# Optimization experiments

Hardware: AMD Instinct MI355X
Metric: run time of the kernel (lower is better)

The kernel has to match this reference:

```python
import jax, jax.numpy as jnp
import numpy as np

H = 2880      # hidden_size
NH = 64       # num query heads
NKV = 8       # num kv heads
D = 64        # head_dim
G = NH // NKV # GQA group size
W = 128       # sliding window (keys per query, incl. self)
THETA = 150000.0
N = 1024      # tokens


def setup_inputs() -> dict:
    key = jax.random.key(0)
    k0, k1, k2, k3 = jax.random.split(key, 4)
    hidden_states = jax.random.normal(k0, (N, H), jnp.float32)
    Wqkv = jax.random.normal(k1, (H, (NH + 2 * NKV) * D), jnp.float32) * (H ** -0.5)
    Wo = jax.random.normal(k2, (NH * D, H), jnp.float32) * ((NH * D) ** -0.5)
    sinks = jax.random.normal(k3, (NH,), jnp.float32)
    positions = jnp.arange(N, dtype=jnp.int64)
    return {"hidden_states": hidden_states, "Wqkv": Wqkv, "Wo": Wo,
            "sinks": sinks, "positions": positions}


def _rope(x, pos):
    # NeoX-style rotary over full head_dim. x: [n, h, D], pos: [n]
    half = D // 2
    inv_freq = 1.0 / (THETA ** (jnp.arange(half, dtype=jnp.float32) / half))
    ang = pos[:, None].astype(jnp.float32) * inv_freq          # [n, half]
    cos = jnp.cos(ang)[:, None, :]
    sin = jnp.sin(ang)[:, None, :]
    x1, x2 = x[..., :half], x[..., half:]
    return jnp.concatenate([x1 * cos - x2 * sin, x2 * cos + x1 * sin], axis=-1)


def reference(hidden_states, Wqkv, Wo, sinks, positions):
    n = hidden_states.shape[0]
    qkv = hidden_states @ Wqkv
    q, k, v = jnp.split(qkv, [NH * D, NH * D + NKV * D], axis=-1)
    q = _rope(q.reshape(n, NH, D), positions)   # [n, NH, D]
    k = _rope(k.reshape(n, NKV, D), positions)  # [n, NKV, D]
    v = v.reshape(n, NKV, D)

    # Sliding-window key indices: query i attends keys j in [i-W+1, i]
    idx = positions[:, None] - (W - 1) + jnp.arange(W)[None, :]  # [n, W]
    valid = idx >= 0
    idx = jnp.clip(idx, 0, n - 1)
    k_win = k[idx]  # [n, W, NKV, D]
    v_win = v[idx]  # [n, W, NKV, D]

    qg = q.reshape(n, NKV, G, D)
    scores = jnp.einsum('nkgd,nwkd->nkgw', qg, k_win) * (D ** -0.5)
    scores = jnp.where(valid[:, None, None, :], scores, -jnp.inf)

    # Attention sinks: softmax over [scores, sink_logit]; sink gets no value.
    sink = sinks.reshape(NKV, G)                      # [NKV, G]
    m = jnp.maximum(scores.max(-1), sink[None])       # [n, NKV, G]
    p = jnp.exp(scores - m[..., None])                # [n, NKV, G, W]
    denom = p.sum(-1) + jnp.exp(sink[None] - m)       # [n, NKV, G]
    out = jnp.einsum('nkgw,nwkd->nkgd', p, v_win) / denom[..., None]
    return out.reshape(n, NH * D) @ Wo
```

## Files before the change

kernel.cpp:

```cpp
#include <hip/hip_runtime.h>
#include <hip/hip_bf16.h>

#define HDIM   2880
#define NH     64
#define NKV    8
#define DHEAD  64
#define GQ     (NH / NKV)
#define WIN    128
#define NTOK   1024
#define QKV_N  ((NH + 2 * NKV) * DHEAD)
#define QCOLS  (NH * DHEAD)
#define KOFF   QCOLS
#define VOFF   (QCOLS + NKV * DHEAD)
#define WO_PAD 2944
#define SK1    3
#define SK2    4

typedef __attribute__((ext_vector_type(8))) short short8;
typedef __attribute__((ext_vector_type(4))) float floatx4;

__device__ unsigned short g_Xb   [(size_t)NTOK  * HDIM];
__device__ unsigned short g_qkvb [(size_t)NTOK  * QKV_N];
__device__ unsigned short g_attn [(size_t)NTOK  * QCOLS];
__device__ unsigned short g_WqkvT[(size_t)QKV_N * HDIM];
__device__ unsigned short g_WoT  [(size_t)WO_PAD * QCOLS];
__device__ float          g_part1[(size_t)SK1 * NTOK * QKV_N];
__device__ float          g_part2[(size_t)SK2 * NTOK * WO_PAD];

__device__ __forceinline__ unsigned short f2b(float f) {
    __hip_bfloat16 h = __float2bfloat16(f);
    return *reinterpret_cast<unsigned short*>(&h);
}

__device__ __forceinline__ void gload_lds16(const unsigned short* g, unsigned short* l) {
    __builtin_amdgcn_global_load_lds(
        (const __attribute__((address_space(1))) unsigned int*)g,
        (__attribute__((address_space(3))) unsigned int*)l, 16, 0, 0);
}

__global__ __launch_bounds__(256) void transpose_cvt(
        const float* __restrict__ in, unsigned short* __restrict__ out,
        int K, int N) {
    int bk = blockIdx.x, bn = blockIdx.y;
    int t = threadIdx.x;
    __shared__ __align__(16) unsigned short T[64 * 72];
    #pragma unroll
    for (int i = 0; i < 4; ++i) {
        int c = i * 256 + t;
        int r = c >> 4, cc = (c & 15) * 4;
        float4 v = *(const float4*)(in + (size_t)(bk * 64 + r) * N + bn * 64 + cc);
        T[r * 72 + cc + 0] = f2b(v.x);
        T[r * 72 + cc + 1] = f2b(v.y);
        T[r * 72 + cc + 2] = f2b(v.z);
        T[r * 72 + cc + 3] = f2b(v.w);
    }
    __syncthreads();
    #pragma unroll
    for (int i = 0; i < 2; ++i) {
        int c = i * 256 + t;
        int rn = c >> 3, kc = (c & 7) * 8;
        int4 vv;
        unsigned short* tp = (unsigned short*)&vv;
        #pragma unroll
        for (int j = 0; j < 8; ++j) tp[j] = T[(kc + j) * 72 + rn];
        *(int4*)(out + (size_t)(bn * 64 + rn) * K + bk * 64 + kc) = vv;
    }
}

__global__ __launch_bounds__(256) void cvt_bf16(
        const float* __restrict__ in, unsigned short* __restrict__ out, int n4) {
    int id = blockIdx.x * 256 + threadIdx.x;
    if (id >= n4) return;
    float4 v = *(const float4*)(in + (size_t)id * 4);
    ushort4 o;
    o.x = f2b(v.x); o.y = f2b(v.y); o.z = f2b(v.z); o.w = f2b(v.w);
    *(ushort4*)(out + (size_t)id * 4) = o;
}

__global__ __launch_bounds__(256) void gemm_sk(
        const unsigned short* __restrict__ A, const unsigned short* __restrict__ Bt,
        float* __restrict__ P, int K, int chunk, int ldc, size_t plane) {
    int bm = blockIdx.x, bn = blockIdx.y, z = blockIdx.z;
    int t = threadIdx.x, lane = t & 63, wid = t >> 6;
    int quad = lane >> 4, ml = lane & 15;
    int wm = wid >> 1, wn = wid & 1;
    __shared__ __align__(16) unsigned short As[128 * 64];
    __shared__ __align__(16) unsigned short Bs[128 * 64];
    floatx4 acc[4][4];
    #pragma unroll
    for (int i = 0; i < 4; ++i)
        #pragma unroll
        for (int j = 0; j < 4; ++j) acc[i][j] = (floatx4){0.f, 0.f, 0.f, 0.f};

    int srow = lane >> 3;
    int scol = (lane & 7) * 8;
    int base = z * chunk;
    const unsigned short* Ab = A  + (size_t)(bm * 128) * K + base;
    const unsigned short* Bb = Bt + (size_t)(bn * 128) * K + base;

    for (int k0 = 0; k0 < chunk; k0 += 64) {
        #pragma unroll
        for (int j = 0; j < 4; ++j) {
            int grp = wid * 4 + j;
            int r = grp * 8 + srow;
            gload_lds16(Ab + (size_t)r * K + k0 + scol, &As[grp * 512]);
            gload_lds16(Bb + (size_t)r * K + k0 + scol, &Bs[grp * 512]);
        }
        __syncthreads();
        #pragma unroll
        for (int kk = 0; kk < 64; kk += 32) {
            short8 af[4], bf[4];
            #pragma unroll
            for (int mt = 0; mt < 4; ++mt)
                af[mt] = *(const short8*)&As[(wm * 64 + mt * 16 + ml) * 64 + kk + quad * 8];
            #pragma unroll
            for (int nt = 0; nt < 4; ++nt)
                bf[nt] = *(const short8*)&Bs[(wn * 64 + nt * 16 + ml) * 64 + kk + quad * 8];
            #pragma unroll
            for (int mt = 0; mt < 4; ++mt)
                #pragma unroll
                for (int nt = 0; nt < 4; ++nt)
                    acc[mt][nt] = __builtin_amdgcn_mfma_f32_16x16x32_bf16(af[mt], bf[nt], acc[mt][nt], 0, 0, 0);
        }
        __syncthreads();
    }
    float* Cp = P + z * plane;
    #pragma unroll
    for (int mt = 0; mt < 4; ++mt)
        #pragma unroll
        for (int nt = 0; nt < 4; ++nt)
            #pragma unroll
            for (int r = 0; r < 4; ++r) {
                int row = bm * 128 + wm * 64 + mt * 16 + quad * 4 + r;
                int col = bn * 128 + wn * 64 + nt * 16 + ml;
                Cp[(size_t)row * ldc + col] = acc[mt][nt][r];
            }
}

#define QK_UNITS (NTOK * 72 * 8)
#define V_UNITS  (NTOK * 128)
__global__ __launch_bounds__(256) void reduce_rope(
        const float* __restrict__ P, unsigned short* __restrict__ qkvb) {
    int id = blockIdx.x * 256 + threadIdx.x;
    const size_t plane = (size_t)NTOK * QKV_N;
    if (id < QK_UNITS) {
        int n = id / 576;
        int rem = id - n * 576;
        int hh = rem >> 3, q8 = rem & 7;
        int c0 = (hh < NH) ? hh * 64 : KOFF + (hh - NH) * 64;
        size_t i1 = (size_t)n * QKV_N + c0 + q8 * 4;
        float4 a0 = *(const float4*)(P + i1);
        float4 a1 = *(const float4*)(P + plane + i1);
        float4 a2 = *(const float4*)(P + 2 * plane + i1);
        float4 b0 = *(const float4*)(P + i1 + 32);
        float4 b1 = *(const float4*)(P + plane + i1 + 32);
        float4 b2 = *(const float4*)(P + 2 * plane + i1 + 32);
        float x1[4] = {a0.x + a1.x + a2.x, a0.y + a1.y + a2.y,
                       a0.z + a1.z + a2.z, a0.w + a1.w + a2.w};
        float x2[4] = {b0.x + b1.x + b2.x, b0.y + b1.y + b2.y,
                       b0.z + b1.z + b2.z, b0.w + b1.w + b2.w};
        union { ushort4 v; unsigned short u[4]; } o1, o2;
        #pragma unroll
        for (int j = 0; j < 4; ++j) {
            int d = q8 * 4 + j;
            float inv = expf(-(float)d * 0.3724497053f);
            float ang = (float)n * inv;
            float s, c;
            sincosf(ang, &s, &c);
            o1.u[j] = f2b(x1[j] * c - x2[j] * s);
            o2.u[j] = f2b(x2[j] * c + x1[j] * s);
        }
        *(ushort4*)(qkvb + i1) = o1.v;
        *(ushort4*)(qkvb + i1 + 32) = o2.v;
    } else if (id < QK_UNITS + V_UNITS) {
        int vid = id - QK_UNITS;
        int n = vid >> 7, s8 = vid & 127;
        size_t i1 = (size_t)n * QKV_N + VOFF + s8 * 4;
        float4 a0 = *(const float4*)(P + i1);
        float4 a1 = *(const float4*)(P + plane + i1);
        float4 a2 = *(const float4*)(P + 2 * plane + i1);
        union { ushort4 v; unsigned short u[4]; } o;
        o.u[0] = f2b(a0.x + a1.x + a2.x);
        o.u[1] = f2b(a0.y + a1.y + a2.y);
        o.u[2] = f2b(a0.z + a1.z + a2.z);
        o.u[3] = f2b(a0.w + a1.w + a2.w);
        *(ushort4*)(qkvb + i1) = o.v;
    }
}

__global__ __launch_bounds__(256) void reduce_out(
        const float* __restrict__ P, float* __restrict__ out) {
    int id = blockIdx.x * 256 + threadIdx.x;
    if (id >= NTOK * (HDIM / 4)) return;
    int n = id / (HDIM / 4);
    int c = (id - n * (HDIM / 4)) * 4;
    const size_t plane = (size_t)NTOK * WO_PAD;
    size_t i = (size_t)n * WO_PAD + c;
    float4 a0 = *(const float4*)(P + i);
    float4 a1 = *(const float4*)(P + plane + i);
    float4 a2 = *(const float4*)(P + 2 * plane + i);
    float4 a3 = *(const float4*)(P + 3 * plane + i);
    float4 s;
    s.x = a0.x + a1.x + a2.x + a3.x;
    s.y = a0.y + a1.y + a2.y + a3.y;
    s.z = a0.z + a1.z + a2.z + a3.z;
    s.w = a0.w + a1.w + a2.w + a3.w;
    *(float4*)(out + (size_t)n * HDIM + c) = s;
}

#define TQ     16
#define WROWS  160
#define KS_LD  72
#define VT_LD  168
#define PS_LD  168

__global__ __launch_bounds__(256) void attn_mfma(
        const unsigned short* __restrict__ qkvb,
        const float* __restrict__ sinks,
        unsigned short* __restrict__ aout) {
    int t0 = blockIdx.x * TQ, kh = blockIdx.y;
    int t = threadIdx.x, lane = t & 63, wid = t >> 6;
    int quad = lane >> 4, ml = lane & 15;
    int wavebase = wid * 32;

    __shared__ __align__(16) unsigned short Ks[WROWS * KS_LD];
    __shared__ __align__(16) unsigned short Vt[DHEAD * VT_LD];
    __shared__ __align__(16) unsigned short Ps[4 * 16 * PS_LD];
    unsigned short* Psw = &Ps[wid * 16 * PS_LD];

    #pragma unroll
    for (int i = 0; i < 5; ++i) {
        int c = i * 256 + t;
        int w = c >> 3, d8 = (c & 7) * 8;
        int r = t0 - 127 + w;
        r = min(max(r, 0), NTOK - 1);
        *(int4*)&Ks[w * KS_LD + d8] =
            *(const int4*)(qkvb + (size_t)r * QKV_N + KOFF + kh * DHEAD + d8);
        int4 vv = *(const int4*)(qkvb + (size_t)r * QKV_N + VOFF + kh * DHEAD + d8);
        const unsigned short* vp = (const unsigned short*)&vv;
        #pragma unroll
        for (int j = 0; j < 8; ++j) Vt[(d8 + j) * VT_LD + w] = vp[j];
    }
    __syncthreads();

    short8 qf[2][2];
    #pragma unroll
    for (int mt = 0; mt < 2; ++mt) {
        int m = wavebase + mt * 16 + ml;
        int tl = m & 15, g = m >> 4;
        const unsigned short* qp = qkvb + (size_t)(t0 + tl) * QKV_N + (kh * GQ + g) * DHEAD;
        #pragma unroll
        for (int kk = 0; kk < 2; ++kk)
            qf[mt][kk] = *(const short8*)(qp + kk * 32 + quad * 8);
    }

    floatx4 S[2][10];
    #pragma unroll
    for (int mt = 0; mt < 2; ++mt)
        #pragma unroll
        for (int nt = 0; nt < 10; ++nt) S[mt][nt] = (floatx4){0.f, 0.f, 0.f, 0.f};
    #pragma unroll
    for (int kk = 0; kk < 2; ++kk) {
        #pragma unroll
        for (int nt = 0; nt < 10; ++nt) {
            short8 kb = *(const short8*)&Ks[(nt * 16 + ml) * KS_LD + kk * 32 + quad * 8];
            #pragma unroll
            for (int mt = 0; mt < 2; ++mt)
                S[mt][nt] = __builtin_amdgcn_mfma_f32_16x16x32_bf16(qf[mt][kk], kb, S[mt][nt], 0, 0, 0);
        }
    }

    int wmin0 = 127 - t0;
    #pragma unroll
    for (int mt = 0; mt < 2; ++mt) {
        #pragma unroll
        for (int r = 0; r < 4; ++r) {
            int tl = (wavebase + mt * 16 + quad * 4 + r) & 15;
            int wlo = tl > wmin0 ? tl : wmin0;
            int whi = tl + 127;
            #pragma unroll
            for (int nt = 0; nt < 10; ++nt) {
                int w = nt * 16 + ml;
                float s = S[mt][nt][r] * 0.125f;
                S[mt][nt][r] = (w >= wlo && w <= whi) ? s : -INFINITY;
            }
        }
    }

    #pragma unroll
    for (int mt = 0; mt < 2; ++mt) {
        int g = (wavebase + mt * 16) >> 4;
        float sk = sinks[kh * GQ + g];
        #pragma unroll
        for (int r = 0; r < 4; ++r) {
            float rm = -INFINITY;
            #pragma unroll
            for (int nt = 0; nt < 10; ++nt) rm = fmaxf(rm, S[mt][nt][r]);
            #pragma unroll
            for (int off = 1; off < 16; off <<= 1) rm = fmaxf(rm, __shfl_xor(rm, off));
            rm = fmaxf(rm, sk);
            float sum = 0.f;
            #pragma unroll
            for (int nt = 0; nt < 10; ++nt) {
                float p = __expf(S[mt][nt][r] - rm);
                S[mt][nt][r] = p;
                sum += p;
            }
            #pragma unroll
            for (int off = 1; off < 16; off <<= 1) sum += __shfl_xor(sum, off);
            float inv = 1.f / (sum + __expf(sk - rm));
            #pragma unroll
            for (int nt = 0; nt < 10; ++nt) S[mt][nt][r] *= inv;
        }
    }

    #pragma unroll
    for (int mt = 0; mt < 2; ++mt) {
        #pragma unroll
        for (int r = 0; r < 4; ++r) {
            int lr = quad * 4 + r;
            #pragma unroll
            for (int nt = 0; nt < 10; ++nt)
                Psw[lr * PS_LD + nt * 16 + ml] = f2b(S[mt][nt][r]);
        }
        floatx4 O[4];
        #pragma unroll
        for (int j = 0; j < 4; ++j) O[j] = (floatx4){0.f, 0.f, 0.f, 0.f};
        #pragma unroll
        for (int ks = 0; ks < 5; ++ks) {
            short8 pf = *(const short8*)&Psw[ml * PS_LD + ks * 32 + quad * 8];
            #pragma unroll
            for (int nt = 0; nt < 4; ++nt) {
                short8 vf = *(const short8*)&Vt[(nt * 16 + ml) * VT_LD + ks * 32 + quad * 8];
                O[nt] = __builtin_amdgcn_mfma_f32_16x16x32_bf16(pf, vf, O[nt], 0, 0, 0);
            }
        }
        #pragma unroll
        for (int r = 0; r < 4; ++r) {
            int mm = wavebase + mt * 16 + quad * 4 + r;
            int tl = mm & 15, g = mm >> 4;
            unsigned short* op = aout + (size_t)(t0 + tl) * QCOLS + (kh * GQ + g) * DHEAD;
            #pragma unroll
            for (int nt = 0; nt < 4; ++nt)
                op[nt * 16 + ml] = f2b(O[nt][r]);
        }
    }
}

extern "C" void kernel_launch(void* const* d_in, const int* in_sizes, int n_in,
                              void* d_out, int out_size, void* d_ws, size_t ws_size,
                              hipStream_t stream) {
    const float* X     = (const float*)d_in[0];
    const float* Wqkv  = (const float*)d_in[1];
    const float* Wo    = (const float*)d_in[2];
    const float* sinks = (const float*)d_in[3];
    float* out = (float*)d_out;

    unsigned short *Xb, *qkvb, *attn, *WqkvT, *WoT;
    float *part1, *part2;
    hipGetSymbolAddress((void**)&Xb,    HIP_SYMBOL(g_Xb));
    hipGetSymbolAddress((void**)&qkvb,  HIP_SYMBOL(g_qkvb));
    hipGetSymbolAddress((void**)&attn,  HIP_SYMBOL(g_attn));
    hipGetSymbolAddress((void**)&WqkvT, HIP_SYMBOL(g_WqkvT));
    hipGetSymbolAddress((void**)&WoT,   HIP_SYMBOL(g_WoT));
    hipGetSymbolAddress((void**)&part1, HIP_SYMBOL(g_part1));
    hipGetSymbolAddress((void**)&part2, HIP_SYMBOL(g_part2));

    cvt_bf16<<<(NTOK * HDIM / 4 + 255) / 256, 256, 0, stream>>>(X, Xb, NTOK * HDIM / 4);
    transpose_cvt<<<dim3(HDIM / 64, QKV_N / 64), 256, 0, stream>>>(Wqkv, WqkvT, HDIM, QKV_N);
    transpose_cvt<<<dim3(QCOLS / 64, HDIM / 64), 256, 0, stream>>>(Wo, WoT, QCOLS, HDIM);

    gemm_sk<<<dim3(NTOK / 128, QKV_N / 128, SK1), 256, 0, stream>>>(
        Xb, WqkvT, part1, HDIM, HDIM / SK1, QKV_N, (size_t)NTOK * QKV_N);

    reduce_rope<<<(QK_UNITS + V_UNITS) / 256, 256, 0, stream>>>(part1, qkvb);

    attn_mfma<<<dim3(NTOK / TQ, NKV), 256, 0, stream>>>(qkvb, sinks, attn);

    gemm_sk<<<dim3(NTOK / 128, WO_PAD / 128, SK2), 256, 0, stream>>>(
        attn, WoT, part2, QCOLS, QCOLS / SK2, WO_PAD, (size_t)NTOK * WO_PAD);

    reduce_out<<<(NTOK * (HDIM / 4) + 255) / 256, 256, 0, stream>>>(part2, out);
}
```

Measured before the change: 330.7 us.

## Replace split-K GEMMs with direct 128x64 tiles and fuse RoPE into epilogue

Drops split-K partial planes and the separate reduce kernels. Each GEMM now computes full K with 128x64 tiles and writes final output directly, with RoPE and the bf16 conversion fused into the QKV GEMM epilogue. Block indices are remapped so consecutive blocks are spread across M tiles, for cache locality and XCD distribution, in both the GEMMs and attention. This removes large fp32 partial traffic and two launches, but the longer K loops have less parallelism (640 and 360 blocks) and no pipelining.

Measured after the change: 315.9 us. 1.05x faster.

```diff
diff --git a/kernel.cpp b/kernel.cpp
--- a/kernel.cpp
+++ b/kernel.cpp
@@ -12,9 +12,6 @@
 #define QCOLS  (NH * DHEAD)
 #define KOFF   QCOLS
 #define VOFF   (QCOLS + NKV * DHEAD)
-#define WO_PAD 2944
-#define SK1    3
-#define SK2    4
 
 typedef __attribute__((ext_vector_type(8))) short short8;
 typedef __attribute__((ext_vector_type(4))) float floatx4;
@@ -23,9 +20,7 @@
 __device__ unsigned short g_qkvb [(size_t)NTOK  * QKV_N];
 __device__ unsigned short g_attn [(size_t)NTOK  * QCOLS];
 __device__ unsigned short g_WqkvT[(size_t)QKV_N * HDIM];
-__device__ unsigned short g_WoT  [(size_t)WO_PAD * QCOLS];
-__device__ float          g_part1[(size_t)SK1 * NTOK * QKV_N];
-__device__ float          g_part2[(size_t)SK2 * NTOK * WO_PAD];
+__device__ unsigned short g_WoT  [(size_t)HDIM * QCOLS];
 
 __device__ __forceinline__ unsigned short f2b(float f) {
     __hip_bfloat16 h = __float2bfloat16(f);
@@ -77,135 +72,108 @@
     *(ushort4*)(out + (size_t)id * 4) = o;
 }
 
-__global__ __launch_bounds__(256) void gemm_sk(
+template<int KLEN, int MODE, int NBN>
+__global__ __launch_bounds__(256) void gemm_dir(
         const unsigned short* __restrict__ A, const unsigned short* __restrict__ Bt,
-        float* __restrict__ P, int K, int chunk, int ldc, size_t plane) {
-    int bm = blockIdx.x, bn = blockIdx.y, z = blockIdx.z;
+        void* __restrict__ outp) {
+    int d0 = blockIdx.x;
+    int work = (d0 & 7) * NBN + (d0 >> 3);
+    int bm = work & 7, bn = work >> 3;
     int t = threadIdx.x, lane = t & 63, wid = t >> 6;
     int quad = lane >> 4, ml = lane & 15;
-    int wm = wid >> 1, wn = wid & 1;
     __shared__ __align__(16) unsigned short As[128 * 64];
-    __shared__ __align__(16) unsigned short Bs[128 * 64];
-    floatx4 acc[4][4];
-    #pragma unroll
-    for (int i = 0; i < 4; ++i)
+    __shared__ __align__(16) unsigned short Bs[64 * 64];
+    floatx4 acc[2][4];
+    #pragma unroll
+    for (int i = 0; i < 2; ++i)
         #pragma unroll
         for (int j = 0; j < 4; ++j) acc[i][j] = (floatx4){0.f, 0.f, 0.f, 0.f};
 
     int srow = lane >> 3;
     int scol = (lane & 7) * 8;
-    int base = z * chunk;
-    const unsigned short* Ab = A  + (size_t)(bm * 128) * K + base;
-    const unsigned short* Bb = Bt + (size_t)(bn * 128) * K + base;
-
-    for (int k0 = 0; k0 < chunk; k0 += 64) {
+    const unsigned short* Ab = A  + (size_t)(bm * 128) * KLEN;
+    const unsigned short* Bb = Bt + (size_t)(bn * 64) * KLEN;
+
+    for (int k0 = 0; k0 < KLEN; k0 += 64) {
         #pragma unroll
         for (int j = 0; j < 4; ++j) {
             int grp = wid * 4 + j;
             int r = grp * 8 + srow;
-            gload_lds16(Ab + (size_t)r * K + k0 + scol, &As[grp * 512]);
-            gload_lds16(Bb + (size_t)r * K + k0 + scol, &Bs[grp * 512]);
+            gload_lds16(Ab + (size_t)r * KLEN + k0 + scol, &As[grp * 512]);
+        }
+        #pragma unroll
+        for (int j = 0; j < 2; ++j) {
+            int grp = wid * 2 + j;
+            int r = grp * 8 + srow;
+            gload_lds16(Bb + (size_t)r * KLEN + k0 + scol, &Bs[grp * 512]);
         }
         __syncthreads();
         #pragma unroll
         for (int kk = 0; kk < 64; kk += 32) {
-            short8 af[4], bf[4];
-            #pragma unroll
-            for (int mt = 0; mt < 4; ++mt)
-                af[mt] = *(const short8*)&As[(wm * 64 + mt * 16 + ml) * 64 + kk + quad * 8];
+            short8 af[2], bf[4];
+            #pragma unroll
+            for (int mt = 0; mt < 2; ++mt)
+                af[mt] = *(const short8*)&As[(wid * 32 + mt * 16 + ml) * 64 + kk + quad * 8];
             #pragma unroll
             for (int nt = 0; nt < 4; ++nt)
-                bf[nt] = *(const short8*)&Bs[(wn * 64 + nt * 16 + ml) * 64 + kk + quad * 8];
-            #pragma unroll
-            for (int mt = 0; mt < 4; ++mt)
+                bf[nt] = *(const short8*)&Bs[(nt * 16 + ml) * 64 + kk + quad * 8];
+            #pragma unroll
+            for (int mt = 0; mt < 2; ++mt)
                 #pragma unroll
                 for (int nt = 0; nt < 4; ++nt)
                     acc[mt][nt] = __builtin_amdgcn_mfma_f32_16x16x32_bf16(af[mt], bf[nt], acc[mt][nt], 0, 0, 0);
         }
         __syncthreads();
     }
-    float* Cp = P + z * plane;
-    #pragma unroll
-    for (int mt = 0; mt < 4; ++mt)
-        #pragma unroll
-        for (int nt = 0; nt < 4; ++nt)
+
+    if constexpr (MODE == 0) {
+        unsigned short* qp = (unsigned short*)outp;
+        int cb = bn * 64;
+        if (bn < NH + NKV) {
+            float inv0 = expf(-(float)ml * 0.3724497053f);
+            float inv1 = expf(-(float)(16 + ml) * 0.3724497053f);
+            #pragma unroll
+            for (int mt = 0; mt < 2; ++mt) {
+                #pragma unroll
+                for (int r = 0; r < 4; ++r) {
+                    int n = bm * 128 + wid * 32 + mt * 16 + quad * 4 + r;
+                    unsigned short* op = qp + (size_t)n * QKV_N + cb;
+                    float s0, c0, s1, c1;
+                    sincosf((float)n * inv0, &s0, &c0);
+                    sincosf((float)n * inv1, &s1, &c1);
+                    float x1a = acc[mt][0][r], x2a = acc[mt][2][r];
+                    float x1b = acc[mt][1][r], x2b = acc[mt][3][r];
+                    op[ml]           = f2b(x1a * c0 - x2a * s0);
+                    op[ml + 32]      = f2b(x2a * c0 + x1a * s0);
+                    op[16 + ml]      = f2b(x1b * c1 - x2b * s1);
+                    op[16 + ml + 32] = f2b(x2b * c1 + x1b * s1);
+                }
+            }
+        } else {
+            #pragma unroll
+            for (int mt = 0; mt < 2; ++mt)
+                #pragma unroll
+                for (int r = 0; r < 4; ++r) {
+                    int n = bm * 128 + wid * 32 + mt * 16 + quad * 4 + r;
+                    unsigned short* op = qp + (size_t)n * QKV_N + cb;
+                    #pragma unroll
+                    for (int nt = 0; nt < 4; ++nt)
+                        op[nt * 16 + ml] = f2b(acc[mt][nt][r]);
+                }
+        }
+    } else {
+        float* op0 = (float*)outp;
+        #pragma unroll
+        for (int mt = 0; mt < 2; ++mt)
             #pragma unroll
             for (int r = 0; r < 4; ++r) {
-                int row = bm * 128 + wm * 64 + mt * 16 + quad * 4 + r;
-                int col = bn * 128 + wn * 64 + nt * 16 + ml;
-                Cp[(size_t)row * ldc + col] = acc[mt][nt][r];
-            }
-}
-
-#define QK_UNITS (NTOK * 72 * 8)
-#define V_UNITS  (NTOK * 128)
-__global__ __launch_bounds__(256) void reduce_rope(
-        const float* __restrict__ P, unsigned short* __restrict__ qkvb) {
-    int id = blockIdx.x * 256 + threadIdx.x;
-    const size_t plane = (size_t)NTOK * QKV_N;
-    if (id < QK_UNITS) {
-        int n = id / 576;
-        int rem = id - n * 576;
-        int hh = rem >> 3, q8 = rem & 7;
-        int c0 = (hh < NH) ? hh * 64 : KOFF + (hh - NH) * 64;
-        size_t i1 = (size_t)n * QKV_N + c0 + q8 * 4;
-        float4 a0 = *(const float4*)(P + i1);
-        float4 a1 = *(const float4*)(P + plane + i1);
-        float4 a2 = *(const float4*)(P + 2 * plane + i1);
-        float4 b0 = *(const float4*)(P + i1 + 32);
-        float4 b1 = *(const float4*)(P + plane + i1 + 32);
-        float4 b2 = *(const float4*)(P + 2 * plane + i1 + 32);
-        float x1[4] = {a0.x + a1.x + a2.x, a0.y + a1.y + a2.y,
-                       a0.z + a1.z + a2.z, a0.w + a1.w + a2.w};
-        float x2[4] = {b0.x + b1.x + b2.x, b0.y + b1.y + b2.y,
-                       b0.z + b1.z + b2.z, b0.w + b1.w + b2.w};
-        union { ushort4 v; unsigned short u[4]; } o1, o2;
-        #pragma unroll
-        for (int j = 0; j < 4; ++j) {
-            int d = q8 * 4 + j;
-            float inv = expf(-(float)d * 0.3724497053f);
-            float ang = (float)n * inv;
-            float s, c;
-            sincosf(ang, &s, &c);
-            o1.u[j] = f2b(x1[j] * c - x2[j] * s);
-            o2.u[j] = f2b(x2[j] * c + x1[j] * s);
-        }
-        *(ushort4*)(qkvb + i1) = o1.v;
-        *(ushort4*)(qkvb + i1 + 32) = o2.v;
-    } else if (id < QK_UNITS + V_UNITS) {
-        int vid = id - QK_UNITS;
-        int n = vid >> 7, s8 = vid & 127;
-        size_t i1 = (size_t)n * QKV_N + VOFF + s8 * 4;
-        float4 a0 = *(const float4*)(P + i1);
-        float4 a1 = *(const float4*)(P + plane + i1);
-        float4 a2 = *(const float4*)(P + 2 * plane + i1);
-        union { ushort4 v; unsigned short u[4]; } o;
-        o.u[0] = f2b(a0.x + a1.x + a2.x);
-        o.u[1] = f2b(a0.y + a1.y + a2.y);
-        o.u[2] = f2b(a0.z + a1.z + a2.z);
-        o.u[3] = f2b(a0.w + a1.w + a2.w);
-        *(ushort4*)(qkvb + i1) = o.v;
-    }
-}
-
-__global__ __launch_bounds__(256) void reduce_out(
-        const float* __restrict__ P, float* __restrict__ out) {
-    int id = blockIdx.x * 256 + threadIdx.x;
-    if (id >= NTOK * (HDIM / 4)) return;
-    int n = id / (HDIM / 4);
-    int c = (id - n * (HDIM / 4)) * 4;
-    const size_t plane = (size_t)NTOK * WO_PAD;
-    size_t i = (size_t)n * WO_PAD + c;
-    float4 a0 = *(const float4*)(P + i);
-    float4 a1 = *(const float4*)(P + plane + i);
-    float4 a2 = *(const float4*)(P + 2 * plane + i);
-    float4 a3 = *(const float4*)(P + 3 * plane + i);
-    float4 s;
-    s.x = a0.x + a1.x + a2.x + a3.x;
-    s.y = a0.y + a1.y + a2.y + a3.y;
-    s.z = a0.z + a1.z + a2.z + a3.z;
-    s.w = a0.w + a1.w + a2.w + a3.w;
-    *(float4*)(out + (size_t)n * HDIM + c) = s;
+                int n = bm * 128 + wid * 32 + mt * 16 + quad * 4 + r;
+                float* op = op0 + (size_t)n * HDIM + bn * 64;
+                #pragma unroll
+                for (int nt = 0; nt < 4; ++nt)
+                    op[nt * 16 + ml] = acc[mt][nt][r];
+            }
+    }
 }
 
 #define TQ     16
@@ -218,7 +186,9 @@
         const unsigned short* __restrict__ qkvb,
         const float* __restrict__ sinks,
         unsigned short* __restrict__ aout) {
-    int t0 = blockIdx.x * TQ, kh = blockIdx.y;
+    int d0 = blockIdx.x;
+    int work = (d0 & 7) * 64 + (d0 >> 3);
+    int t0 = (work & 63) * TQ, kh = work >> 6;
     int t = threadIdx.x, lane = t & 63, wid = t >> 6;
     int quad = lane >> 4, ml = lane & 15;
     int wavebase = wid * 32;
@@ -357,28 +327,19 @@
     float* out = (float*)d_out;
 
     unsigned short *Xb, *qkvb, *attn, *WqkvT, *WoT;
-    float *part1, *part2;
     hipGetSymbolAddress((void**)&Xb,    HIP_SYMBOL(g_Xb));
     hipGetSymbolAddress((void**)&qkvb,  HIP_SYMBOL(g_qkvb));
     hipGetSymbolAddress((void**)&attn,  HIP_SYMBOL(g_attn));
     hipGetSymbolAddress((void**)&WqkvT, HIP_SYMBOL(g_WqkvT));
     hipGetSymbolAddress((void**)&WoT,   HIP_SYMBOL(g_WoT));
-    hipGetSymbolAddress((void**)&part1, HIP_SYMBOL(g_part1));
-    hipGetSymbolAddress((void**)&part2, HIP_SYMBOL(g_part2));
 
     cvt_bf16<<<(NTOK * HDIM / 4 + 255) / 256, 256, 0, stream>>>(X, Xb, NTOK * HDIM / 4);
     transpose_cvt<<<dim3(HDIM / 64, QKV_N / 64), 256, 0, stream>>>(Wqkv, WqkvT, HDIM, QKV_N);
     transpose_cvt<<<dim3(QCOLS / 64, HDIM / 64), 256, 0, stream>>>(Wo, WoT, QCOLS, HDIM);
 
-    gemm_sk<<<dim3(NTOK / 128, QKV_N / 128, SK1), 256, 0, stream>>>(
-        Xb, WqkvT, part1, HDIM, HDIM / SK1, QKV_N, (size_t)NTOK * QKV_N);
-
-    reduce_rope<<<(QK_UNITS + V_UNITS) / 256, 256, 0, stream>>>(part1, qkvb);
-
-    attn_mfma<<<dim3(NTOK / TQ, NKV), 256, 0, stream>>>(qkvb, sinks, attn);
-
-    gemm_sk<<<dim3(NTOK / 128, WO_PAD / 128, SK2), 256, 0, stream>>>(
-        attn, WoT, part2, QCOLS, QCOLS / SK2, WO_PAD, (size_t)NTOK * WO_PAD);
-
-    reduce_out<<<(NTOK * (HDIM / 4) + 255) / 256, 256, 0, stream>>>(part2, out);
-}
+    gemm_dir<HDIM, 0, QKV_N / 64><<<8 * (QKV_N / 64), 256, 0, stream>>>(Xb, WqkvT, qkvb);
+
+    attn_mfma<<<512, 256, 0, stream>>>(qkvb, sinks, attn);
+
+    gemm_dir<QCOLS, 1, HDIM / 64><<<8 * (HDIM / 64), 256, 0, stream>>>(attn, WoT, out);
+}
```
